# Optimization experiments

Hardware: AMD Instinct MI355X
Metric: run time of the kernel (lower is better)

Reference implementation:

```python
import jax, jax.numpy as jnp
import numpy as np
from jax import lax

IN_CH = 256
FILTERS_PER_CH = 2            # expansion = 1 -> 2 filters per input channel
INTER_CH = IN_CH * FILTERS_PER_CH
BUTTERFLY_SIZE = 8
BUTTERFLIES = INTER_CH // 2 // BUTTERFLY_SIZE  # 32
WING = BUTTERFLY_SIZE // 2                      # 4


def setup_inputs() -> dict:
    key = jax.random.key(0)
    k1, k2 = jax.random.split(key)
    x = jax.random.normal(k1, (32, IN_CH, 56, 56), dtype=jnp.float32)
    # depthwise conv weight, PyTorch OIHW with groups=IN_CH: (INTER_CH, 1, 3, 3)
    w = jax.random.normal(k2, (INTER_CH, 1, 3, 3), dtype=jnp.float32) * 0.1
    return {"x": x, "w": w}


def reference(x, w):
    # grouped (depthwise, channel multiplier 2) conv, stride 1, pad 1, no bias
    y = lax.conv_general_dilated(
        x, w,
        window_strides=(1, 1),
        padding=[(1, 1), (1, 1)],
        feature_group_count=IN_CH,
        dimension_numbers=("NCHW", "OIHW", "NCHW"),
    )  # (B, INTER_CH, H, W); channels group-major: 2i,2i+1 from input i
    B, C2, H, W = y.shape
    # extract_sequences: consecutive channels alternate between the two outputs
    y = y.reshape(B, C2 // 2, 2, H, W)
    x1 = y[:, :, 0]  # (B, IN_CH, H, W)
    x2 = y[:, :, 1]
    # swap_wings: within each butterfly, swap the two wings
    s = x2.reshape(B, BUTTERFLIES, 2, WING, H, W)
    x2 = jnp.flip(s, axis=2).reshape(B, C2 // 2, H, W)
    return x1 + x2
```

## Files before the change

kernel.cpp:

```cpp
#include <hip/hip_runtime.h>

#define IN_CH 256
#define IMG_H 56
#define IMG_W 56
#define BAND_ROWS 28
#define LDS_W 60
#define LDS_H 30
#define CH_ELEMS (LDS_W * LDS_H)

__global__ __launch_bounds__(256, 6) void dwconv_butterfly(
    const float* __restrict__ x, const float* __restrict__ wgt,
    float* __restrict__ out)
{
    __shared__ float lds[2 * CH_ELEMS];

    const int tid  = threadIdx.x;
    const int p    = blockIdx.x;
    const int b    = blockIdx.y;
    const int band = blockIdx.z;
    const int c0   = ((p >> 2) << 3) | (p & 3);
    const int c1   = c0 ^ 4;

    const size_t chan = (size_t)IMG_H * IMG_W;
    const float* x0 = x + ((size_t)b * IN_CH + c0) * chan;
    const float* x1 = x + ((size_t)b * IN_CH + c1) * chan;
    float* o0 = out + ((size_t)b * IN_CH + c0) * chan + (size_t)band * BAND_ROWS * IMG_W;
    float* o1 = out + ((size_t)b * IN_CH + c1) * chan + (size_t)band * BAND_ROWS * IMG_W;

    const int gbase  = band ? 27 : 0;
    const int lrbase = band ? 0 : 1;

    float4 v[3];
    int    ofs[3];
#pragma unroll
    for (int k = 0; k < 3; ++k) {
        const int q    = tid + 256 * k;
        const int ch   = (q >= 406) ? 1 : 0;
        const int rem  = q - ch * 406;
        const int row  = rem / 14;
        const int colq = rem - row * 14;
        const float* src = (ch ? x1 : x0) + (gbase + row) * IMG_W + colq * 4;
        v[k]   = *(const float4*)src;
        ofs[k] = ch * CH_ELEMS + (lrbase + row) * LDS_W + colq * 4 + 1;
    }
    float4 v3; int ofs3 = 0; const bool has3 = (tid < 44);
    if (has3) {
        const int q    = 768 + tid;
        const int rem  = q - 406;
        const int row  = rem / 14;
        const int colq = rem - row * 14;
        v3   = *(const float4*)(x1 + (gbase + row) * IMG_W + colq * 4);
        ofs3 = CH_ELEMS + (lrbase + row) * LDS_W + colq * 4 + 1;
    }

    if (tid < 236) {
        const int ch = tid / 118;
        const int r  = tid - ch * 118;
        int row, col;
        if (r < 58) { row = band ? (LDS_H - 1) : 0; col = r; }
        else        { const int rr = r - 58; row = rr >> 1; col = (rr & 1) ? (LDS_W - 3) : 0; }
        lds[ch * CH_ELEMS + row * LDS_W + col] = 0.f;
    }

#pragma unroll
    for (int k = 0; k < 3; ++k) {
        float* d = &lds[ofs[k]];
        d[0] = v[k].x; d[1] = v[k].y; d[2] = v[k].z; d[3] = v[k].w;
    }
    if (has3) {
        float* d = &lds[ofs3];
        d[0] = v3.x; d[1] = v3.y; d[2] = v3.z; d[3] = v3.w;
    }

    __syncthreads();

    float wa[9], wb[9], wc[9], wd[9];
    {
        const float* pa = wgt + (size_t)(2 * c0) * 9;
        const float* pb = wgt + (size_t)(2 * c1 + 1) * 9;
        const float* pc = wgt + (size_t)(2 * c1) * 9;
        const float* pd = wgt + (size_t)(2 * c0 + 1) * 9;
#pragma unroll
        for (int i = 0; i < 9; ++i) {
            wa[i] = pa[i]; wb[i] = pb[i]; wc[i] = pc[i]; wd[i] = pd[i];
        }
    }

    auto compute_quad = [&](int idx) {
        const int h  = idx / 14;
        const int w0 = (idx - h * 14) * 4;
        float acc0[4] = {0.f, 0.f, 0.f, 0.f};
        float acc1[4] = {0.f, 0.f, 0.f, 0.f};
#pragma unroll
        for (int kh = 0; kh < 3; ++kh) {
            const float* p0 = &lds[(h + kh) * LDS_W + w0];
            const float* p1 = p0 + CH_ELEMS;
            const float4 a0 = *(const float4*)p0;
            const float2 b0 = *(const float2*)(p0 + 4);
            const float4 a1 = *(const float4*)p1;
            const float2 b1 = *(const float2*)(p1 + 4);
            const float r0[6] = {a0.x, a0.y, a0.z, a0.w, b0.x, b0.y};
            const float r1[6] = {a1.x, a1.y, a1.z, a1.w, b1.x, b1.y};
#pragma unroll
            for (int kw = 0; kw < 3; ++kw) {
                const float fa = wa[kh * 3 + kw], fb = wb[kh * 3 + kw];
                const float fc = wc[kh * 3 + kw], fd = wd[kh * 3 + kw];
#pragma unroll
                for (int i = 0; i < 4; ++i) {
                    acc0[i] += r0[i + kw] * fa + r1[i + kw] * fb;
                    acc1[i] += r1[i + kw] * fc + r0[i + kw] * fd;
                }
            }
        }
        *(float4*)(o0 + h * IMG_W + w0) = make_float4(acc0[0], acc0[1], acc0[2], acc0[3]);
        *(float4*)(o1 + h * IMG_W + w0) = make_float4(acc1[0], acc1[1], acc1[2], acc1[3]);
    };

    compute_quad(tid);
    if (tid < 136) compute_quad(256 + tid);
}

extern "C" void kernel_launch(void* const* d_in, const int* in_sizes, int n_in,
                              void* d_out, int out_size, void* d_ws, size_t ws_size,
                              hipStream_t stream) {
    const float* x = (const float*)d_in[0];
    const float* w = (const float*)d_in[1];
    float* out = (float*)d_out;

    dim3 grid(IN_CH / 2, 32, 2);
    dim3 block(256);
    dwconv_butterfly<<<grid, block, 0, stream>>>(x, w, out);
}
```

Baseline: 184.9 us.

## Load input tiles directly into LDS and compute two output rows per thread

Input rows are copied straight from global memory into LDS with the global_load_lds builtin, using an unpadded layout, instead of passing through registers. Zero-padding moves into predicated register selects. Each thread now computes a 2-row by 4-column output patch from a 4-row register window, which reuses the loaded rows vertically. The aim is to cut VGPR staging, LDS write instructions and redundant LDS reads. The cost is that only 196 of 256 threads do compute work, and the code depends on the per-wave LDS placement semantics of global_load_lds being correct, in particular the tail store for tid<44.

New measurement: 186.8 us. Within noise of the previous version (+1.0%).

```diff
diff --git a/kernel.cpp b/kernel.cpp
--- a/kernel.cpp
+++ b/kernel.cpp
@@ -1,18 +1,19 @@
 #include <hip/hip_runtime.h>
 
 #define IN_CH 256
-#define IMG_H 56
 #define IMG_W 56
-#define BAND_ROWS 28
-#define LDS_W 60
-#define LDS_H 30
-#define CH_ELEMS (LDS_W * LDS_H)
+#define BAND  28
+#define LROWS 29
+#define CH_F  (LROWS * IMG_W)
+
+typedef __attribute__((address_space(1))) const void GBuf;
+typedef __attribute__((address_space(3))) void LBuf;
 
 __global__ __launch_bounds__(256, 6) void dwconv_butterfly(
     const float* __restrict__ x, const float* __restrict__ wgt,
     float* __restrict__ out)
 {
-    __shared__ float lds[2 * CH_ELEMS];
+    __shared__ float lds[2 * CH_F];
 
     const int tid  = threadIdx.x;
     const int p    = blockIdx.x;
@@ -21,58 +22,31 @@
     const int c0   = ((p >> 2) << 3) | (p & 3);
     const int c1   = c0 ^ 4;
 
-    const size_t chan = (size_t)IMG_H * IMG_W;
+    const size_t chan = 56u * 56u;
     const float* x0 = x + ((size_t)b * IN_CH + c0) * chan;
     const float* x1 = x + ((size_t)b * IN_CH + c1) * chan;
-    float* o0 = out + ((size_t)b * IN_CH + c0) * chan + (size_t)band * BAND_ROWS * IMG_W;
-    float* o1 = out + ((size_t)b * IN_CH + c1) * chan + (size_t)band * BAND_ROWS * IMG_W;
+    float* o0 = out + ((size_t)b * IN_CH + c0) * chan + (size_t)band * BAND * IMG_W;
+    float* o1 = out + ((size_t)b * IN_CH + c1) * chan + (size_t)band * BAND * IMG_W;
 
-    const int gbase  = band ? 27 : 0;
-    const int lrbase = band ? 0 : 1;
+    const int gbase = band ? 27 : 0;
+    const float* g0 = x0 + gbase * IMG_W;
+    const float* g1 = x1 + gbase * IMG_W;
 
-    float4 v[3];
-    int    ofs[3];
+    {
+        const int wbase = tid & ~63;
 #pragma unroll
-    for (int k = 0; k < 3; ++k) {
-        const int q    = tid + 256 * k;
-        const int ch   = (q >= 406) ? 1 : 0;
-        const int rem  = q - ch * 406;
-        const int row  = rem / 14;
-        const int colq = rem - row * 14;
-        const float* src = (ch ? x1 : x0) + (gbase + row) * IMG_W + colq * 4;
-        v[k]   = *(const float4*)src;
-        ofs[k] = ch * CH_ELEMS + (lrbase + row) * LDS_W + colq * 4 + 1;
+        for (int k = 0; k < 3; ++k) {
+            const int q = tid + 256 * k;
+            const float* src = (q < 406) ? (g0 + 4 * q) : (g1 + 4 * (q - 406));
+            __builtin_amdgcn_global_load_lds((GBuf*)src,
+                (LBuf*)&lds[4 * (256 * k + wbase)], 16, 0, 0);
+        }
+        if (tid < 44) {
+            const float* src = g1 + 4 * (768 + tid - 406);
+            __builtin_amdgcn_global_load_lds((GBuf*)src,
+                (LBuf*)&lds[4 * 768], 16, 0, 0);
+        }
     }
-    float4 v3; int ofs3 = 0; const bool has3 = (tid < 44);
-    if (has3) {
-        const int q    = 768 + tid;
-        const int rem  = q - 406;
-        const int row  = rem / 14;
-        const int colq = rem - row * 14;
-        v3   = *(const float4*)(x1 + (gbase + row) * IMG_W + colq * 4);
-        ofs3 = CH_ELEMS + (lrbase + row) * LDS_W + colq * 4 + 1;
-    }
-
-    if (tid < 236) {
-        const int ch = tid / 118;
-        const int r  = tid - ch * 118;
-        int row, col;
-        if (r < 58) { row = band ? (LDS_H - 1) : 0; col = r; }
-        else        { const int rr = r - 58; row = rr >> 1; col = (rr & 1) ? (LDS_W - 3) : 0; }
-        lds[ch * CH_ELEMS + row * LDS_W + col] = 0.f;
-    }
-
-#pragma unroll
-    for (int k = 0; k < 3; ++k) {
-        float* d = &lds[ofs[k]];
-        d[0] = v[k].x; d[1] = v[k].y; d[2] = v[k].z; d[3] = v[k].w;
-    }
-    if (has3) {
-        float* d = &lds[ofs3];
-        d[0] = v3.x; d[1] = v3.y; d[2] = v3.z; d[3] = v3.w;
-    }
-
-    __syncthreads();
 
     float wa[9], wb[9], wc[9], wd[9];
     {
@@ -86,38 +60,81 @@
         }
     }
 
-    auto compute_quad = [&](int idx) {
-        const int h  = idx / 14;
-        const int w0 = (idx - h * 14) * 4;
-        float acc0[4] = {0.f, 0.f, 0.f, 0.f};
-        float acc1[4] = {0.f, 0.f, 0.f, 0.f};
+    __syncthreads();
+
+    if (tid < 196) {
+        const int rp  = tid / 14;
+        const int w0  = (tid - rp * 14) * 4;
+        const int oh0 = rp * 2;
+        const int rbase = oh0 - 1 + band;
+
+        const bool has_l = (w0 > 0);
+        const bool has_r = (w0 < 52);
+        const int  col_l = has_l ? (w0 - 1) : 0;
+        const int  col_r = has_r ? (w0 + 4) : 55;
+
+        float W[4][12];
 #pragma unroll
-        for (int kh = 0; kh < 3; ++kh) {
-            const float* p0 = &lds[(h + kh) * LDS_W + w0];
-            const float* p1 = p0 + CH_ELEMS;
+        for (int rr = 0; rr < 4; ++rr) {
+            const int r  = rbase + rr;
+            const bool zr = (rr == 0) ? (r < 0) : ((rr == 3) ? (r > 28) : false);
+            const int  rc = (rr == 0) ? (r < 0 ? 0 : r) : ((rr == 3) ? (r > 28 ? 28 : r) : r);
+            const float* p0 = &lds[rc * IMG_W + w0];
+            const float* p1 = p0 + CH_F;
             const float4 a0 = *(const float4*)p0;
-            const float2 b0 = *(const float2*)(p0 + 4);
             const float4 a1 = *(const float4*)p1;
-            const float2 b1 = *(const float2*)(p1 + 4);
-            const float r0[6] = {a0.x, a0.y, a0.z, a0.w, b0.x, b0.y};
-            const float r1[6] = {a1.x, a1.y, a1.z, a1.w, b1.x, b1.y};
+            const float l0 = lds[rc * IMG_W + col_l];
+            const float r0 = lds[rc * IMG_W + col_r];
+            const float l1 = lds[CH_F + rc * IMG_W + col_l];
+            const float r1 = lds[CH_F + rc * IMG_W + col_r];
+            W[rr][0]  = (zr || !has_l) ? 0.f : l0;
+            W[rr][1]  = zr ? 0.f : a0.x;
+            W[rr][2]  = zr ? 0.f : a0.y;
+            W[rr][3]  = zr ? 0.f : a0.z;
+            W[rr][4]  = zr ? 0.f : a0.w;
+            W[rr][5]  = (zr || !has_r) ? 0.f : r0;
+            W[rr][6]  = (zr || !has_l) ? 0.f : l1;
+            W[rr][7]  = zr ? 0.f : a1.x;
+            W[rr][8]  = zr ? 0.f : a1.y;
+            W[rr][9]  = zr ? 0.f : a1.z;
+            W[rr][10] = zr ? 0.f : a1.w;
+            W[rr][11] = (zr || !has_r) ? 0.f : r1;
+        }
+
+        float acc[2][8];
 #pragma unroll
-            for (int kw = 0; kw < 3; ++kw) {
-                const float fa = wa[kh * 3 + kw], fb = wb[kh * 3 + kw];
-                const float fc = wc[kh * 3 + kw], fd = wd[kh * 3 + kw];
+        for (int j = 0; j < 2; ++j)
 #pragma unroll
-                for (int i = 0; i < 4; ++i) {
-                    acc0[i] += r0[i + kw] * fa + r1[i + kw] * fb;
-                    acc1[i] += r1[i + kw] * fc + r0[i + kw] * fd;
+            for (int i = 0; i < 8; ++i) acc[j][i] = 0.f;
+
+#pragma unroll
+        for (int j = 0; j < 2; ++j) {
+#pragma unroll
+            for (int kh = 0; kh < 3; ++kh) {
+                const int rw = j + kh;
+#pragma unroll
+                for (int kw = 0; kw < 3; ++kw) {
+                    const float fa = wa[kh * 3 + kw], fb = wb[kh * 3 + kw];
+                    const float fc = wc[kh * 3 + kw], fd = wd[kh * 3 + kw];
+#pragma unroll
+                    for (int i = 0; i < 4; ++i) {
+                        const float u0 = W[rw][i + kw];
+                        const float u1 = W[rw][6 + i + kw];
+                        acc[j][i]     += u0 * fa + u1 * fb;
+                        acc[j][4 + i] += u1 * fc + u0 * fd;
+                    }
                 }
             }
         }
-        *(float4*)(o0 + h * IMG_W + w0) = make_float4(acc0[0], acc0[1], acc0[2], acc0[3]);
-        *(float4*)(o1 + h * IMG_W + w0) = make_float4(acc1[0], acc1[1], acc1[2], acc1[3]);
-    };
 
-    compute_quad(tid);
-    if (tid < 136) compute_quad(256 + tid);
+#pragma unroll
+        for (int j = 0; j < 2; ++j) {
+            float* q0 = o0 + (oh0 + j) * IMG_W + w0;
+            float* q1 = o1 + (oh0 + j) * IMG_W + w0;
+            *(float4*)q0 = make_float4(acc[j][0], acc[j][1], acc[j][2], acc[j][3]);
+            *(float4*)q1 = make_float4(acc[j][4], acc[j][5], acc[j][6], acc[j][7]);
+        }
+    }
 }
 
 extern "C" void kernel_launch(void* const* d_in, const int* in_sizes, int n_in,
```

## Stage per-wave row slabs via direct global-to-LDS loads, drop block barrier

Applied to the files above, without the earlier changes.

Each wave now loads its own 9-row halo slab for both channels straight into a private LDS region using global_load_lds, instead of staging the whole band through registers and padded LDS. Halo padding is replaced by clamped addresses plus masking of edge values in registers. The block-wide __syncthreads goes away, leaving only a vmcnt wait. Outputs use nontemporal stores and the occupancy hint rises to 8. Each wave re-reads two overlapping halo rows and adds select logic, and the lack of an explicit LDS-visibility wait beyond vmcnt is a correctness risk.

After: 195.9 us. +5.9%, slower.

```diff
diff --git a/kernel.cpp b/kernel.cpp
--- a/kernel.cpp
+++ b/kernel.cpp
@@ -1,78 +1,49 @@
 #include <hip/hip_runtime.h>
 
 #define IN_CH 256
-#define IMG_H 56
 #define IMG_W 56
-#define BAND_ROWS 28
-#define LDS_W 60
-#define LDS_H 30
-#define CH_ELEMS (LDS_W * LDS_H)
+#define CH_FLOATS 3136
 
-__global__ __launch_bounds__(256, 6) void dwconv_butterfly(
+typedef __attribute__((address_space(1))) const void GBuf;
+typedef __attribute__((address_space(3))) void LBuf;
+typedef float f4 __attribute__((ext_vector_type(4)));
+
+__global__ __launch_bounds__(256, 8) void dwconv_butterfly(
     const float* __restrict__ x, const float* __restrict__ wgt,
     float* __restrict__ out)
 {
-    __shared__ float lds[2 * CH_ELEMS];
+    __shared__ float lds[4 * 1024];
 
     const int tid  = threadIdx.x;
+    const int lane = tid & 63;
+    const int w    = tid >> 6;
     const int p    = blockIdx.x;
     const int b    = blockIdx.y;
     const int band = blockIdx.z;
     const int c0   = ((p >> 2) << 3) | (p & 3);
     const int c1   = c0 ^ 4;
 
-    const size_t chan = (size_t)IMG_H * IMG_W;
-    const float* x0 = x + ((size_t)b * IN_CH + c0) * chan;
-    const float* x1 = x + ((size_t)b * IN_CH + c1) * chan;
-    float* o0 = out + ((size_t)b * IN_CH + c0) * chan + (size_t)band * BAND_ROWS * IMG_W;
-    float* o1 = out + ((size_t)b * IN_CH + c1) * chan + (size_t)band * BAND_ROWS * IMG_W;
+    const float* x0 = x + ((size_t)b * IN_CH + c0) * CH_FLOATS;
+    const float* x1 = x + ((size_t)b * IN_CH + c1) * CH_FLOATS;
+    float* o0 = out + ((size_t)b * IN_CH + c0) * CH_FLOATS;
+    float* o1 = out + ((size_t)b * IN_CH + c1) * CH_FLOATS;
 
-    const int gbase  = band ? 27 : 0;
-    const int lrbase = band ? 0 : 1;
+    const int obase  = band * 28 + 7 * w;
+    const int wstart = obase - 1;
 
-    float4 v[3];
-    int    ofs[3];
+    float* const wlds = &lds[w * 1024];
 #pragma unroll
-    for (int k = 0; k < 3; ++k) {
-        const int q    = tid + 256 * k;
-        const int ch   = (q >= 406) ? 1 : 0;
-        const int rem  = q - ch * 406;
-        const int row  = rem / 14;
-        const int colq = rem - row * 14;
-        const float* src = (ch ? x1 : x0) + (gbase + row) * IMG_W + colq * 4;
-        v[k]   = *(const float4*)src;
-        ofs[k] = ch * CH_ELEMS + (lrbase + row) * LDS_W + colq * 4 + 1;
+    for (int ch = 0; ch < 2; ++ch) {
+        const float* xc = ch ? x1 : x0;
+#pragma unroll
+        for (int i = 0; i < 2; ++i) {
+            const int k  = i * 64 + lane;
+            int fidx = wstart * IMG_W + 4 * k;
+            fidx = fidx < 0 ? 0 : (fidx > CH_FLOATS - 4 ? CH_FLOATS - 4 : fidx);
+            __builtin_amdgcn_global_load_lds((GBuf*)(xc + fidx),
+                (LBuf*)&wlds[ch * 512 + i * 256], 16, 0, 0);
+        }
     }
-    float4 v3; int ofs3 = 0; const bool has3 = (tid < 44);
-    if (has3) {
-        const int q    = 768 + tid;
-        const int rem  = q - 406;
-        const int row  = rem / 14;
-        const int colq = rem - row * 14;
-        v3   = *(const float4*)(x1 + (gbase + row) * IMG_W + colq * 4);
-        ofs3 = CH_ELEMS + (lrbase + row) * LDS_W + colq * 4 + 1;
-    }
-
-    if (tid < 236) {
-        const int ch = tid / 118;
-        const int r  = tid - ch * 118;
-        int row, col;
-        if (r < 58) { row = band ? (LDS_H - 1) : 0; col = r; }
-        else        { const int rr = r - 58; row = rr >> 1; col = (rr & 1) ? (LDS_W - 3) : 0; }
-        lds[ch * CH_ELEMS + row * LDS_W + col] = 0.f;
-    }
-
-#pragma unroll
-    for (int k = 0; k < 3; ++k) {
-        float* d = &lds[ofs[k]];
-        d[0] = v[k].x; d[1] = v[k].y; d[2] = v[k].z; d[3] = v[k].w;
-    }
-    if (has3) {
-        float* d = &lds[ofs3];
-        d[0] = v3.x; d[1] = v3.y; d[2] = v3.z; d[3] = v3.w;
-    }
-
-    __syncthreads();
 
     float wa[9], wb[9], wc[9], wd[9];
     {
@@ -86,38 +57,75 @@
         }
     }
 
-    auto compute_quad = [&](int idx) {
-        const int h  = idx / 14;
-        const int w0 = (idx - h * 14) * 4;
-        float acc0[4] = {0.f, 0.f, 0.f, 0.f};
-        float acc1[4] = {0.f, 0.f, 0.f, 0.f};
+    asm volatile("s_waitcnt vmcnt(0)" ::: "memory");
+    __builtin_amdgcn_sched_barrier(0);
+
 #pragma unroll
-        for (int kh = 0; kh < 3; ++kh) {
-            const float* p0 = &lds[(h + kh) * LDS_W + w0];
-            const float* p1 = p0 + CH_ELEMS;
-            const float4 a0 = *(const float4*)p0;
-            const float2 b0 = *(const float2*)(p0 + 4);
-            const float4 a1 = *(const float4*)p1;
-            const float2 b1 = *(const float2*)(p1 + 4);
-            const float r0[6] = {a0.x, a0.y, a0.z, a0.w, b0.x, b0.y};
-            const float r1[6] = {a1.x, a1.y, a1.z, a1.w, b1.x, b1.y};
+    for (int pass = 0; pass < 2; ++pass) {
+        const int u = lane + 64 * pass;
+        if (u < 98) {
+            const int r  = u / 14;
+            const int s  = u - r * 14;
+            const int w0 = 4 * s;
+            const bool has_l = (s > 0);
+            const bool has_r = (s < 13);
+            const int  col_l = has_l ? w0 - 1 : 0;
+            const int  col_r = has_r ? w0 + 4 : 55;
+
+            float W[3][12];
 #pragma unroll
-            for (int kw = 0; kw < 3; ++kw) {
-                const float fa = wa[kh * 3 + kw], fb = wb[kh * 3 + kw];
-                const float fc = wc[kh * 3 + kw], fd = wd[kh * 3 + kw];
+            for (int kh = 0; kh < 3; ++kh) {
+                const int  l  = r + kh;
+                const bool zr = (band == 0 && w == 0 && l == 0) ||
+                                (band == 1 && w == 3 && l == 8);
+                const float* p0 = &wlds[l * IMG_W + w0];
+                const float* p1 = p0 + 512;
+                const f4 a0 = *(const f4*)p0;
+                const f4 a1 = *(const f4*)p1;
+                const float l0 = wlds[l * IMG_W + col_l];
+                const float r0 = wlds[l * IMG_W + col_r];
+                const float l1 = wlds[512 + l * IMG_W + col_l];
+                const float r1 = wlds[512 + l * IMG_W + col_r];
+                W[kh][0]  = (zr || !has_l) ? 0.f : l0;
+                W[kh][1]  = zr ? 0.f : a0.x;
+                W[kh][2]  = zr ? 0.f : a0.y;
+                W[kh][3]  = zr ? 0.f : a0.z;
+                W[kh][4]  = zr ? 0.f : a0.w;
+                W[kh][5]  = (zr || !has_r) ? 0.f : r0;
+                W[kh][6]  = (zr || !has_l) ? 0.f : l1;
+                W[kh][7]  = zr ? 0.f : a1.x;
+                W[kh][8]  = zr ? 0.f : a1.y;
+                W[kh][9]  = zr ? 0.f : a1.z;
+                W[kh][10] = zr ? 0.f : a1.w;
+                W[kh][11] = (zr || !has_r) ? 0.f : r1;
+            }
+
+            float acc[8];
 #pragma unroll
-                for (int i = 0; i < 4; ++i) {
-                    acc0[i] += r0[i + kw] * fa + r1[i + kw] * fb;
-                    acc1[i] += r1[i + kw] * fc + r0[i + kw] * fd;
+            for (int i = 0; i < 8; ++i) acc[i] = 0.f;
+#pragma unroll
+            for (int kh = 0; kh < 3; ++kh) {
+#pragma unroll
+                for (int kw = 0; kw < 3; ++kw) {
+                    const float fa = wa[kh * 3 + kw], fb = wb[kh * 3 + kw];
+                    const float fc = wc[kh * 3 + kw], fd = wd[kh * 3 + kw];
+#pragma unroll
+                    for (int i = 0; i < 4; ++i) {
+                        const float u0 = W[kh][i + kw];
+                        const float u1 = W[kh][6 + i + kw];
+                        acc[i]     += u0 * fa + u1 * fb;
+                        acc[4 + i] += u1 * fc + u0 * fd;
+                    }
                 }
             }
+
+            const int orow = obase + r;
+            f4 v0; v0.x = acc[0]; v0.y = acc[1]; v0.z = acc[2]; v0.w = acc[3];
+            f4 v1; v1.x = acc[4]; v1.y = acc[5]; v1.z = acc[6]; v1.w = acc[7];
+            __builtin_nontemporal_store(v0, (f4*)(o0 + orow * IMG_W + w0));
+            __builtin_nontemporal_store(v1, (f4*)(o1 + orow * IMG_W + w0));
         }
-        *(float4*)(o0 + h * IMG_W + w0) = make_float4(acc0[0], acc0[1], acc0[2], acc0[3]);
-        *(float4*)(o1 + h * IMG_W + w0) = make_float4(acc1[0], acc1[1], acc1[2], acc1[3]);
-    };
-
-    compute_quad(tid);
-    if (tid < 136) compute_quad(256 + tid);
+    }
 }
 
 extern "C" void kernel_launch(void* const* d_in, const int* in_sizes, int n_in,
```
